# Kernel optimization log

Measured on AMD Instinct MI355X. Metric: run time of the kernel, lower is better.

The kernel has to match this reference:

```python
import jax, jax.numpy as jnp
import numpy as np

HARD_RATIO = 0.5
HARD_WEIGHT = 0.5
B, Q, D = 1024, 32, 512


def _l2norm(x):
    return x / jnp.linalg.norm(x, axis=-1, keepdims=True)


def setup_inputs() -> dict:
    key = jax.random.key(0)
    k1, k2 = jax.random.split(key)
    fusion_feats = _l2norm(jax.random.normal(k1, (B, D), dtype=jnp.float32))
    target_feats = _l2norm(jax.random.normal(k2, (B, Q, D), dtype=jnp.float32))
    temp = jnp.float32(0.07)
    return {"fusion_feats": fusion_feats, "target_feats": target_feats, "temp": temp}


def reference(fusion_feats, target_feats, temp):
    b = fusion_feats.shape[0]
    # sim[i, j, q] = fusion[i] . target[j, q]  -> max over query tokens q
    sim = jnp.einsum('id,jqd->ijq', fusion_feats, target_feats)  # (B, B, Q)
    sim_max = jnp.max(sim, axis=-1) / temp                        # (B, B)

    # standard InfoNCE with diagonal labels
    loss_standard = -jnp.mean(jnp.diagonal(jax.nn.log_softmax(sim_max, axis=-1)))

    # online hard-negative mining: per-row top-k over off-diagonal entries
    num_hard = max(1, int(b * HARD_RATIO))
    diag_mask = jnp.eye(b, dtype=bool)
    masked = jnp.where(diag_mask, -jnp.inf, sim_max)
    hard_sims, _ = jax.lax.top_k(masked, num_hard)                # (B, num_hard)
    pos = jnp.diagonal(sim_max)                                    # (B,)
    # -log(exp(pos) / (exp(pos) + sum exp(hard))) = logsumexp([pos, hard]) - pos
    lse = jax.nn.logsumexp(jnp.concatenate([pos[:, None], hard_sims], axis=1), axis=1)
    hard_loss_online = jnp.mean(lse - pos)

    total_loss = loss_standard + HARD_WEIGHT * hard_loss_online
    return total_loss
```

## Files before the change

kernel.cpp:

```cpp
#include <hip/hip_runtime.h>
#include <hip/hip_bf16.h>
#include <math.h>

typedef unsigned short u16;
typedef unsigned char u8;
typedef unsigned int u32;
typedef long long i64;
typedef __attribute__((ext_vector_type(4))) float f32x4;

__global__ void cvt_fused(const float* __restrict__ F, const float* __restrict__ T,
                          u32* __restrict__ Fb, u32* __restrict__ Tb,
                          float* __restrict__ out) {
    const int idx = blockIdx.x * blockDim.x + threadIdx.x;
    if (idx == 0) out[0] = 0.f;
    const float* s;
    u32* d;
    int i;
    if (idx < 65536) { s = F; d = Fb; i = idx; }
    else             { s = T; d = Tb; i = idx - 65536; }
    const float4 v0 = *(const float4*)(s + (size_t)i * 8);
    const float4 v1 = *(const float4*)(s + (size_t)i * 8 + 4);
    int lo = __builtin_amdgcn_cvt_pk_fp8_f32(v0.x * 16.f, v0.y * 16.f, 0, false);
    lo     = __builtin_amdgcn_cvt_pk_fp8_f32(v0.z * 16.f, v0.w * 16.f, lo, true);
    int hi = __builtin_amdgcn_cvt_pk_fp8_f32(v1.x * 16.f, v1.y * 16.f, 0, false);
    hi     = __builtin_amdgcn_cvt_pk_fp8_f32(v1.z * 16.f, v1.w * 16.f, hi, true);
    uint2 o; o.x = (u32)lo; o.y = (u32)hi;
    const int r  = i >> 6;
    const int ob = (i & 63) << 3;
    const int t  = ob >> 7;
    const int ss = (ob >> 5) & 3;
    const int f  = (ob >> 3) & 3;
    const int o2 = (t << 7) | (f << 5) | (ss << 3);
    ((uint2*)d)[r * 64 + (o2 >> 3)] = o;
}

#define GLB_AS __attribute__((address_space(1)))
#define LDS_AS __attribute__((address_space(3)))

__device__ __forceinline__ void gload_lds16(const void* g, void* l) {
    __builtin_amdgcn_global_load_lds((const GLB_AS void*)g, (LDS_AS void*)l, 16, 0, 0);
}

__device__ __forceinline__ i64 half0(int4 v) { int2 p; p.x = v.x; p.y = v.y; return __builtin_bit_cast(i64, p); }
__device__ __forceinline__ i64 half1(int4 v) { int2 p; p.x = v.z; p.y = v.w; return __builtin_bit_cast(i64, p); }

__global__ __launch_bounds__(256, 4)
void gemm_max(const u8* __restrict__ A, const u8* __restrict__ B,
              const float* __restrict__ temp_ptr, float* __restrict__ sim) {
    __shared__ __align__(16) u8 lA[128 * 128];
    __shared__ __align__(16) u8 lB[128 * 128];
    const int bid = blockIdx.x;
    const int bn  = ((bid & 7) << 5) | ((bid >> 3) & 31);
    const int bm  = bid >> 8;
    const int tid  = threadIdx.x;
    const int wave = tid >> 6;
    const int lane = tid & 63;
    const int wm = wave >> 1;
    const int wn = wave & 1;

    f32x4 acc[4][4] = {};

    const int srow = lane >> 3;
    const int aoff = srow * 512 + (((lane & 7) ^ srow) << 4);
    const u8* gA = A + (size_t)(bm * 128) * 512 + aoff;
    const u8* gB = B + (size_t)(bn * 128) * 512 + aoff;

    const int frow = lane & 15;
    const int fq   = lane >> 4;
    const int r7   = frow & 7;

    for (int k0 = 0; k0 < 512; k0 += 128) {
#pragma unroll
        for (int g = 0; g < 4; ++g)
            gload_lds16(gA + (wave + 4 * g) * 4096 + k0, lA + (wave + 4 * g) * 1024);
#pragma unroll
        for (int g = 0; g < 4; ++g)
            gload_lds16(gB + (wave + 4 * g) * 4096 + k0, lB + (wave + 4 * g) * 1024);
        __syncthreads();

#pragma unroll
        for (int sp = 0; sp < 2; ++sp) {
            const int coff = (((fq << 1) + sp) ^ r7) << 4;
            int4 aF[4], bF[4];
#pragma unroll
            for (int mt = 0; mt < 4; ++mt)
                aF[mt] = *(const int4*)&lA[(wm * 64 + mt * 16 + frow) * 128 + coff];
#pragma unroll
            for (int nt = 0; nt < 4; ++nt)
                bF[nt] = *(const int4*)&lB[(wn * 64 + nt * 16 + frow) * 128 + coff];
#pragma unroll
            for (int mt = 0; mt < 4; ++mt)
#pragma unroll
                for (int nt = 0; nt < 4; ++nt) {
                    acc[mt][nt] = __builtin_amdgcn_mfma_f32_16x16x32_fp8_fp8(
                        half0(aF[mt]), half0(bF[nt]), acc[mt][nt], 0, 0, 0);
                    acc[mt][nt] = __builtin_amdgcn_mfma_f32_16x16x32_fp8_fp8(
                        half1(aF[mt]), half1(bF[nt]), acc[mt][nt], 0, 0, 0);
                }
        }
        __syncthreads();
    }

    const float inv = 1.0f / (256.0f * (*temp_ptr));
    const int jb = (bn * 128 + wn * 64) >> 5;
#pragma unroll
    for (int mt = 0; mt < 4; ++mt) {
#pragma unroll
        for (int rr = 0; rr < 4; ++rr) {
            float v0 = fmaxf(acc[mt][0][rr], acc[mt][1][rr]);
            float v1 = fmaxf(acc[mt][2][rr], acc[mt][3][rr]);
#pragma unroll
            for (int off = 1; off < 16; off <<= 1) {
                v0 = fmaxf(v0, __shfl_xor(v0, off));
                v1 = fmaxf(v1, __shfl_xor(v1, off));
            }
            if ((lane & 15) == 0) {
                const int row = bm * 128 + wm * 64 + mt * 16 + fq * 4 + rr;
                sim[row * 1024 + jb]     = v0 * inv;
                sim[row * 1024 + jb + 1] = v1 * inv;
            }
        }
    }
}

__device__ __forceinline__ u32 f2key(float x) {
    u32 b = __float_as_uint(x);
    return (b & 0x80000000u) ? ~b : (b | 0x80000000u);
}
__device__ __forceinline__ float key2f(u32 k) {
    return __uint_as_float((k & 0x80000000u) ? (k & 0x7fffffffu) : ~k);
}

__global__ __launch_bounds__(256)
void row_loss(const float* __restrict__ sim, float* __restrict__ out) {
    const int tid = threadIdx.x;
    const int lane = tid & 63;
    const int wv = tid >> 6;
    const int i = blockIdx.x * 4 + wv;

    float v[16];
    const float4* rp = (const float4*)(sim + (size_t)i * 1024);
#pragma unroll
    for (int t = 0; t < 4; ++t) {
        float4 f = rp[t * 64 + lane];
        v[t * 4 + 0] = f.x; v[t * 4 + 1] = f.y; v[t * 4 + 2] = f.z; v[t * 4 + 3] = f.w;
    }

    const int dslot = ((i >> 8) << 2) | (i & 3);
    const int dlane = (i >> 2) & 63;

    u32 k[16];
#pragma unroll
    for (int t = 0; t < 16; ++t) {
        u32 kk = f2key(v[t]);
        k[t] = (lane == dlane && t == dslot) ? 0u : kk;
    }

    float pv = 0.f;
#pragma unroll
    for (int t = 0; t < 16; ++t) if (t == dslot) pv = v[t];
    const float pos = __shfl(pv, dlane);

    float m = v[0];
#pragma unroll
    for (int t = 1; t < 16; ++t) m = fmaxf(m, v[t]);
#pragma unroll
    for (int off = 32; off > 0; off >>= 1) m = fmaxf(m, __shfl_xor(m, off));
    float s = 0.f;
#pragma unroll
    for (int t = 0; t < 16; ++t) s += __expf(v[t] - m);
#pragma unroll
    for (int off = 32; off > 0; off >>= 1) s += __shfl_xor(s, off);
    const float loss_std = m + __logf(s) - pos;

    u32 lo = 0u, hi = 0xFFFFFFFFu;
    while (lo < hi) {
        const u32 span = hi - lo;
        const u32 mid = lo + (span >> 1) + (span & 1u);
        int cnt = 0;
#pragma unroll
        for (int t = 0; t < 16; ++t) cnt += (k[t] >= mid);
#pragma unroll
        for (int off = 32; off > 0; off >>= 1) cnt += __shfl_xor(cnt, off);
        if (cnt >= 512) lo = mid; else hi = mid - 1;
    }
    const u32 t_key = lo;
    const float tval = key2f(t_key);

    float se = 0.f;
    int cgt = 0;
#pragma unroll
    for (int t = 0; t < 16; ++t) {
        if (k[t] > t_key) { se += __expf(v[t] - m); ++cgt; }
    }
#pragma unroll
    for (int off = 32; off > 0; off >>= 1) se += __shfl_xor(se, off);
#pragma unroll
    for (int off = 32; off > 0; off >>= 1) cgt += __shfl_xor(cgt, off);

    const float sh = se + (float)(512 - cgt) * __expf(tval - m) + __expf(pos - m);
    const float hard = m + __logf(sh) - pos;

    if (lane == 0)
        atomicAdd(out, (loss_std + 0.5f * hard) * (1.0f / 1024.0f));
}

extern "C" void kernel_launch(void* const* d_in, const int* in_sizes, int n_in,
                              void* d_out, int out_size, void* d_ws, size_t ws_size,
                              hipStream_t stream) {
    const float* F    = (const float*)d_in[0];
    const float* T    = (const float*)d_in[1];
    const float* temp = (const float*)d_in[2];
    float* out = (float*)d_out;

    char* ws = (char*)d_ws;
    u32*  Fb8 = (u32*)ws;
    u32*  Tb8 = (u32*)(ws + (1u << 20));
    float* sim = (float*)(ws + (1u << 20) + (32u << 20));

    cvt_fused<<<8448, 256, 0, stream>>>(F, T, Fb8, Tb8, out);

    gemm_max<<<2048, 256, 0, stream>>>((const u8*)Fb8, (const u8*)Tb8, temp, sim);

    row_loss<<<256, 256, 0, stream>>>(sim, out);
}
```

Measured before the change: 154.5 us.

## Double-buffer LDS tiles in fp8 GEMM to overlap global loads with MFMA

Turns the single-buffered K loop into a two-stage LDS ping-pong. The next K tile is issued via global_load_lds while MFMAs run on the current one, and explicit vmcnt/lgkmcnt waits and barriers replace __syncthreads. It also raises wave priority around the MFMA block. The cost is double the LDS footprint (64KB per block) and launch bounds dropping from 4 to 2 blocks per CU, so occupancy falls.

```diff
diff --git a/kernel.cpp b/kernel.cpp
--- a/kernel.cpp
+++ b/kernel.cpp
@@ -44,11 +44,11 @@
 __device__ __forceinline__ i64 half0(int4 v) { int2 p; p.x = v.x; p.y = v.y; return __builtin_bit_cast(i64, p); }
 __device__ __forceinline__ i64 half1(int4 v) { int2 p; p.x = v.z; p.y = v.w; return __builtin_bit_cast(i64, p); }
 
-__global__ __launch_bounds__(256, 4)
+__global__ __launch_bounds__(256, 2)
 void gemm_max(const u8* __restrict__ A, const u8* __restrict__ B,
               const float* __restrict__ temp_ptr, float* __restrict__ sim) {
-    __shared__ __align__(16) u8 lA[128 * 128];
-    __shared__ __align__(16) u8 lB[128 * 128];
+    __shared__ __align__(16) u8 lA[2][128 * 128];
+    __shared__ __align__(16) u8 lB[2][128 * 128];
     const int bid = blockIdx.x;
     const int bn  = ((bid & 7) << 5) | ((bid >> 3) & 31);
     const int bm  = bid >> 8;
@@ -69,37 +69,59 @@
     const int fq   = lane >> 4;
     const int r7   = frow & 7;
 
-    for (int k0 = 0; k0 < 512; k0 += 128) {
-#pragma unroll
-        for (int g = 0; g < 4; ++g)
-            gload_lds16(gA + (wave + 4 * g) * 4096 + k0, lA + (wave + 4 * g) * 1024);
-#pragma unroll
-        for (int g = 0; g < 4; ++g)
-            gload_lds16(gB + (wave + 4 * g) * 4096 + k0, lB + (wave + 4 * g) * 1024);
-        __syncthreads();
-
+#define STAGE(pb, k0) do {                                                              \
+        _Pragma("unroll")                                                               \
+        for (int g = 0; g < 4; ++g)                                                     \
+            gload_lds16(gA + (wave + 4 * g) * 4096 + (k0), &lA[pb][(wave + 4 * g) * 1024]); \
+        _Pragma("unroll")                                                               \
+        for (int g = 0; g < 4; ++g)                                                     \
+            gload_lds16(gB + (wave + 4 * g) * 4096 + (k0), &lB[pb][(wave + 4 * g) * 1024]); \
+    } while (0)
+
+    STAGE(0, 0);
+    STAGE(1, 128);
+
+#pragma unroll
+    for (int t = 0; t < 4; ++t) {
+        if (t < 3) asm volatile("s_waitcnt vmcnt(8)" ::: "memory");
+        else       asm volatile("s_waitcnt vmcnt(0)" ::: "memory");
+        asm volatile("s_barrier" ::: "memory");
+
+        const int pb = t & 1;
+        int4 aF[2][4], bF[2][4];
 #pragma unroll
         for (int sp = 0; sp < 2; ++sp) {
             const int coff = (((fq << 1) + sp) ^ r7) << 4;
-            int4 aF[4], bF[4];
 #pragma unroll
             for (int mt = 0; mt < 4; ++mt)
-                aF[mt] = *(const int4*)&lA[(wm * 64 + mt * 16 + frow) * 128 + coff];
+                aF[sp][mt] = *(const int4*)&lA[pb][(wm * 64 + mt * 16 + frow) * 128 + coff];
 #pragma unroll
             for (int nt = 0; nt < 4; ++nt)
-                bF[nt] = *(const int4*)&lB[(wn * 64 + nt * 16 + frow) * 128 + coff];
+                bF[sp][nt] = *(const int4*)&lB[pb][(wn * 64 + nt * 16 + frow) * 128 + coff];
+        }
+
+        if (t < 2) {
+            asm volatile("s_waitcnt lgkmcnt(0)" ::: "memory");
+            __builtin_amdgcn_sched_barrier(0);
+            asm volatile("s_barrier" ::: "memory");
+            STAGE(pb, (t + 2) * 128);
+        }
+
+        __builtin_amdgcn_s_setprio(1);
+#pragma unroll
+        for (int sp = 0; sp < 2; ++sp)
 #pragma unroll
             for (int mt = 0; mt < 4; ++mt)
 #pragma unroll
                 for (int nt = 0; nt < 4; ++nt) {
                     acc[mt][nt] = __builtin_amdgcn_mfma_f32_16x16x32_fp8_fp8(
-                        half0(aF[mt]), half0(bF[nt]), acc[mt][nt], 0, 0, 0);
+                        half0(aF[sp][mt]), half0(bF[sp][nt]), acc[mt][nt], 0, 0, 0);
                     acc[mt][nt] = __builtin_amdgcn_mfma_f32_16x16x32_fp8_fp8(
-                        half1(aF[mt]), half1(bF[nt]), acc[mt][nt], 0, 0, 0);
+                        half1(aF[sp][mt]), half1(bF[sp][nt]), acc[mt][nt], 0, 0, 0);
                 }
-        }
-        __syncthreads();
-    }
+        __builtin_amdgcn_s_setprio(0);
+    }
+#undef STAGE
 
     const float inv = 1.0f / (256.0f * (*temp_ptr));
     const int jb = (bn * 128 + wn * 64) >> 5;
```

New measurement: 163.9 us. 6.1% more time.

## Double-buffer LDS tiles in fp8 GEMM-max with prefetch and MFMA priority

Applied to the files above, without the earlier changes.

The GEMM-max kernel now splits each K step into two LDS buffers of 64-wide K chunks and prefetches the next chunk while the current one feeds the MFMAs. This replaces the load-sync-compute-sync pattern with a single barrier per step. It also uses a new swizzled row-pair layout for the LDS fragments and raises wave priority around the MFMA block with s_setprio. LDS footprint stays the same, but the new index mapping must cover K exactly, which adds a correctness risk.

```diff
diff --git a/kernel.cpp b/kernel.cpp
--- a/kernel.cpp
+++ b/kernel.cpp
@@ -47,8 +47,8 @@
 __global__ __launch_bounds__(256, 4)
 void gemm_max(const u8* __restrict__ A, const u8* __restrict__ B,
               const float* __restrict__ temp_ptr, float* __restrict__ sim) {
-    __shared__ __align__(16) u8 lA[128 * 128];
-    __shared__ __align__(16) u8 lB[128 * 128];
+    __shared__ __align__(16) u8 lA[2][128 * 64];
+    __shared__ __align__(16) u8 lB[2][128 * 64];
     const int bid = blockIdx.x;
     const int bn  = ((bid & 7) << 5) | ((bid >> 3) & 31);
     const int bm  = bid >> 8;
@@ -60,46 +60,56 @@
 
     f32x4 acc[4][4] = {};
 
-    const int srow = lane >> 3;
-    const int aoff = srow * 512 + (((lane & 7) ^ srow) << 4);
-    const u8* gA = A + (size_t)(bm * 128) * 512 + aoff;
-    const u8* gB = B + (size_t)(bn * 128) * 512 + aoff;
+    const int pl   = lane >> 3;
+    const int sl   = lane & 7;
+    const int uu   = sl ^ pl;
+    const int stoff = (2 * pl + (uu >> 2)) * 512 + ((uu & 3) << 5);
+    const u8* gA2 = A + (size_t)(bm * 128) * 512 + stoff;
+    const u8* gB2 = B + (size_t)(bn * 128) * 512 + stoff;
 
     const int frow = lane & 15;
     const int fq   = lane >> 4;
-    const int r7   = frow & 7;
-
-    for (int k0 = 0; k0 < 512; k0 += 128) {
-#pragma unroll
-        for (int g = 0; g < 4; ++g)
-            gload_lds16(gA + (wave + 4 * g) * 4096 + k0, lA + (wave + 4 * g) * 1024);
-#pragma unroll
-        for (int g = 0; g < 4; ++g)
-            gload_lds16(gB + (wave + 4 * g) * 4096 + k0, lB + (wave + 4 * g) * 1024);
+    const int prr  = frow >> 1;
+    const int slotr = ((((frow & 1) << 2) + fq) ^ prr) << 4;
+    const int prA = (wm * 32 + prr) * 128 + slotr;
+    const int prB = (wn * 32 + prr) * 128 + slotr;
+
+#define STAGE(pb, t) do {                                                            \
+        const int kt = 128 * ((t) >> 1) + 16 * ((t) & 1);                            \
+        gload_lds16(gA2 + (wave)     * 8192 + kt, &lA[pb][(wave)     * 1024]);       \
+        gload_lds16(gA2 + (wave + 4) * 8192 + kt, &lA[pb][(wave + 4) * 1024]);       \
+        gload_lds16(gB2 + (wave)     * 8192 + kt, &lB[pb][(wave)     * 1024]);       \
+        gload_lds16(gB2 + (wave + 4) * 8192 + kt, &lB[pb][(wave + 4) * 1024]);       \
+    } while (0)
+
+    STAGE(0, 0);
+#pragma unroll
+    for (int t = 0; t < 8; ++t) {
         __syncthreads();
-
-#pragma unroll
-        for (int sp = 0; sp < 2; ++sp) {
-            const int coff = (((fq << 1) + sp) ^ r7) << 4;
-            int4 aF[4], bF[4];
-#pragma unroll
-            for (int mt = 0; mt < 4; ++mt)
-                aF[mt] = *(const int4*)&lA[(wm * 64 + mt * 16 + frow) * 128 + coff];
-#pragma unroll
-            for (int nt = 0; nt < 4; ++nt)
-                bF[nt] = *(const int4*)&lB[(wn * 64 + nt * 16 + frow) * 128 + coff];
-#pragma unroll
-            for (int mt = 0; mt < 4; ++mt)
-#pragma unroll
-                for (int nt = 0; nt < 4; ++nt) {
-                    acc[mt][nt] = __builtin_amdgcn_mfma_f32_16x16x32_fp8_fp8(
-                        half0(aF[mt]), half0(bF[nt]), acc[mt][nt], 0, 0, 0);
-                    acc[mt][nt] = __builtin_amdgcn_mfma_f32_16x16x32_fp8_fp8(
-                        half1(aF[mt]), half1(bF[nt]), acc[mt][nt], 0, 0, 0);
-                }
-        }
-        __syncthreads();
-    }
+        if (t < 7) STAGE((t + 1) & 1, t + 1);
+        const int pb = t & 1;
+
+        int4 aF[4], bF[4];
+#pragma unroll
+        for (int mt = 0; mt < 4; ++mt)
+            aF[mt] = *(const int4*)&lA[pb][prA + mt * 1024];
+#pragma unroll
+        for (int nt = 0; nt < 4; ++nt)
+            bF[nt] = *(const int4*)&lB[pb][prB + nt * 1024];
+
+        __builtin_amdgcn_s_setprio(1);
+#pragma unroll
+        for (int mt = 0; mt < 4; ++mt)
+#pragma unroll
+            for (int nt = 0; nt < 4; ++nt) {
+                acc[mt][nt] = __builtin_amdgcn_mfma_f32_16x16x32_fp8_fp8(
+                    half0(aF[mt]), half0(bF[nt]), acc[mt][nt], 0, 0, 0);
+                acc[mt][nt] = __builtin_amdgcn_mfma_f32_16x16x32_fp8_fp8(
+                    half1(aF[mt]), half1(bF[nt]), acc[mt][nt], 0, 0, 0);
+            }
+        __builtin_amdgcn_s_setprio(0);
+    }
+#undef STAGE
 
     const float inv = 1.0f / (256.0f * (*temp_ptr));
     const int jb = (bn * 128 + wn * 64) >> 5;
```

New measurement: 155.9 us. Within noise of the previous version (+0.9%).
